# Kernel tuning notes

Hardware: AMD Instinct MI355X
Metric: run time of the kernel (lower is better)

The kernel has to match this reference:

```python
import jax, jax.numpy as jnp
import numpy as np

N_NODES = 10000
N_EDGES = 160000
IN_DIM = 256
HEADS = 8
C0 = 32   # per-head out channels, layer 0 (256 // 8)
C1 = 32   # per-head out channels, layer 1 (= output_dim)
RANK = 8
LORA_SCALE = 32.0 / 8      # alpha / rank
ATT_RANK = 4               # rank // 2
ATT_SCALE = 32.0 / 4       # alpha / (rank // 2)
NEG_SLOPE = 0.2


def _gat_layer(x, src, dst, W, A, B, att_s, att_d, As, Bs, Ad, Bd, concat):
    """One LoRAGATConv layer (eval mode, dropout=0)."""
    N = x.shape[0]
    H, C = att_s.shape
    # LoRA-adapted projection: base + B(A x) * scaling -> [N, H, C]
    xp = (x @ W.T + ((x @ A.T) @ B.T) * LORA_SCALE).reshape(N, H, C)

    def att_score(base, Aa, Ba):
        # per-head base dot product + LoRA(out_channels -> 1) path -> [N, H]
        return jnp.einsum('nhc,hc->nh', xp, base) + ((xp @ Aa.T) @ Ba.T)[..., 0] * ATT_SCALE

    s_src = att_score(att_s, As, Bs)  # applied to x_i (destination), per original code
    s_dst = att_score(att_d, Ad, Bd)  # applied to x_j (source), per original code

    alpha = s_src[dst] + s_dst[src]              # [E, H]
    alpha = jax.nn.leaky_relu(alpha, NEG_SLOPE)
    # segment softmax over destination nodes (every node has a self-loop)
    m = jax.ops.segment_max(alpha, dst, num_segments=N)
    e = jnp.exp(alpha - m[dst])
    den = jax.ops.segment_sum(e, dst, num_segments=N)
    a = e / den[dst]                             # [E, H]

    msg = xp[src] * a[:, :, None]                # [E, H, C]
    out = jax.ops.segment_sum(msg, dst, num_segments=N)  # [N, H, C]
    return out.reshape(N, H * C) if concat else out.mean(axis=1)


def _forward(x, edge_index,
             W0, A0, B0, att_src0, att_dst0, Asrc0, Bsrc0, Adst0, Bdst0,
             W1, A1, B1, att_src1, att_dst1, Asrc1, Bsrc1, Adst1, Bdst1):
    N = x.shape[0]
    loops = jnp.arange(N, dtype=edge_index.dtype)
    ei = jnp.concatenate([edge_index, jnp.stack([loops, loops])], axis=1)
    src, dst = ei[0], ei[1]
    h = _gat_layer(x, src, dst, W0, A0, B0, att_src0, att_dst0, Asrc0, Bsrc0, Adst0, Bdst0, concat=True)
    h = jax.nn.elu(h)
    out = _gat_layer(h, src, dst, W1, A1, B1, att_src1, att_dst1, Asrc1, Bsrc1, Adst1, Bdst1, concat=False)
    return out


def setup_inputs() -> dict:
    key = jax.random.key(0)
    ks = jax.random.split(key, 24)
    s = 0.05
    inp = {
        'x': jax.random.normal(ks[0], (N_NODES, IN_DIM), dtype=jnp.float32),
        'edge_index': jax.random.randint(ks[1], (2, N_EDGES), 0, N_NODES, dtype=jnp.int64),
    }
    # layer 0: in 256 -> heads*C0 = 256
    inp['W0'] = jax.random.normal(ks[2], (HEADS * C0, IN_DIM), dtype=jnp.float32) * s
    inp['A0'] = jax.random.normal(ks[3], (RANK, IN_DIM), dtype=jnp.float32) * s
    inp['B0'] = jax.random.normal(ks[4], (HEADS * C0, RANK), dtype=jnp.float32) * s
    inp['att_src0'] = jax.random.normal(ks[5], (HEADS, C0), dtype=jnp.float32) * s
    inp['att_dst0'] = jax.random.normal(ks[6], (HEADS, C0), dtype=jnp.float32) * s
    inp['Asrc0'] = jax.random.normal(ks[7], (ATT_RANK, C0), dtype=jnp.float32) * s
    inp['Bsrc0'] = jax.random.normal(ks[8], (1, ATT_RANK), dtype=jnp.float32) * s
    inp['Adst0'] = jax.random.normal(ks[9], (ATT_RANK, C0), dtype=jnp.float32) * s
    inp['Bdst0'] = jax.random.normal(ks[10], (1, ATT_RANK), dtype=jnp.float32) * s
    # layer 1: in heads*C0 = 256 -> heads*C1 = 256 (head-averaged -> 32)
    D1 = HEADS * C0
    inp['W1'] = jax.random.normal(ks[11], (HEADS * C1, D1), dtype=jnp.float32) * s
    inp['A1'] = jax.random.normal(ks[12], (RANK, D1), dtype=jnp.float32) * s
    inp['B1'] = jax.random.normal(ks[13], (HEADS * C1, RANK), dtype=jnp.float32) * s
    inp['att_src1'] = jax.random.normal(ks[14], (HEADS, C1), dtype=jnp.float32) * s
    inp['att_dst1'] = jax.random.normal(ks[15], (HEADS, C1), dtype=jnp.float32) * s
    inp['Asrc1'] = jax.random.normal(ks[16], (ATT_RANK, C1), dtype=jnp.float32) * s
    inp['Bsrc1'] = jax.random.normal(ks[17], (1, ATT_RANK), dtype=jnp.float32) * s
    inp['Adst1'] = jax.random.normal(ks[18], (ATT_RANK, C1), dtype=jnp.float32) * s
    inp['Bdst1'] = jax.random.normal(ks[19], (1, ATT_RANK), dtype=jnp.float32) * s
    return inp


def reference(x, edge_index,
              W0, A0, B0, att_src0, att_dst0, Asrc0, Bsrc0, Adst0, Bdst0,
              W1, A1, B1, att_src1, att_dst1, Asrc1, Bsrc1, Adst1, Bdst1):
    return _forward(x, edge_index,
                    W0, A0, B0, att_src0, att_dst0, Asrc0, Bsrc0, Adst0, Bdst0,
                    W1, A1, B1, att_src1, att_dst1, Asrc1, Bsrc1, Adst1, Bdst1)
```

## Files before the change

### kernel.cpp

```cpp
#include <hip/hip_runtime.h>

#define LORA_SCALE 4.0f
#define ATT_SCALE 8.0f
#define NEG_SLOPE 0.2f
#define ELLW 64

typedef __attribute__((ext_vector_type(8))) short bf16x8;
typedef __attribute__((ext_vector_type(4))) float f32x4;
typedef unsigned short ushort_t;
typedef unsigned int uint_t;

__device__ inline ushort_t f2bf(float f) {
    uint_t u = __float_as_uint(f);
    u += 0x7fff + ((u >> 16) & 1);
    return (ushort_t)(u >> 16);
}
__device__ inline float bf2f(ushort_t h) {
    return __uint_as_float(((uint_t)h) << 16);
}
__device__ inline void split_bf(float f, ushort_t& h, ushort_t& l) {
    h = f2bf(f);
    l = f2bf(f - bf2f(h));
}

__global__ void prep_all(const float* __restrict__ W0, const float* __restrict__ A0,
                         const float* __restrict__ B0,
                         const float* __restrict__ att_s0, const float* __restrict__ att_d0,
                         const float* __restrict__ As0, const float* __restrict__ Bs0,
                         const float* __restrict__ Ad0, const float* __restrict__ Bd0,
                         const float* __restrict__ W1, const float* __restrict__ A1,
                         const float* __restrict__ B1,
                         const float* __restrict__ att_s1, const float* __restrict__ att_d1,
                         const float* __restrict__ As1, const float* __restrict__ Bs1,
                         const float* __restrict__ Ad1, const float* __restrict__ Bd1,
                         ushort_t* __restrict__ whi0, ushort_t* __restrict__ wlo0,
                         ushort_t* __restrict__ whi1, ushort_t* __restrict__ wlo1,
                         float* __restrict__ effS0, float* __restrict__ effD0,
                         float* __restrict__ effS1, float* __restrict__ effD1,
                         const float* __restrict__ x, ushort_t* __restrict__ xhi,
                         ushort_t* __restrict__ xlo,
                         const int* __restrict__ ei, int E_real, int E_total,
                         int* __restrict__ cnt, int* __restrict__ ell, int N)
{
    int b = blockIdx.x;
    int t = threadIdx.x;
    if (b < 512) {
        int layer = b >> 8;
        int i = (b & 255) * 256 + t;
        const float* W = layer ? W1 : W0;
        const float* A = layer ? A1 : A0;
        const float* B = layer ? B1 : B0;
        int r = i >> 8, c = i & 255;
        float acc = W[i];
        #pragma unroll
        for (int k = 0; k < 8; k++) acc += LORA_SCALE * B[r * 8 + k] * A[k * 256 + c];
        ushort_t h, l;
        split_bf(acc, h, l);
        if (layer) { whi1[i] = h; wlo1[i] = l; }
        else       { whi0[i] = h; wlo0[i] = l; }
        if (i < 256) {
            int c2 = i & 31;
            const float* as_ = layer ? att_s1 : att_s0;
            const float* ad_ = layer ? att_d1 : att_d0;
            const float* As = layer ? As1 : As0;
            const float* Bs = layer ? Bs1 : Bs0;
            const float* Ad = layer ? Ad1 : Ad0;
            const float* Bd = layer ? Bd1 : Bd0;
            float es = as_[i], ed = ad_[i];
            #pragma unroll
            for (int k = 0; k < 4; k++) {
                es += ATT_SCALE * Bs[k] * As[k * 32 + c2];
                ed += ATT_SCALE * Bd[k] * Ad[k * 32 + c2];
            }
            if (layer) { effS1[i] = es; effD1[i] = ed; }
            else       { effS0[i] = es; effD0[i] = ed; }
        }
        return;
    }
    int cb = b - 512;
    int convB = (N * 32 + 255) / 256;
    if (cb < convB) {
        int i = cb * 256 + t;
        if (i >= N * 32) return;
        float4 v0 = *(const float4*)(x + i * 8);
        float4 v1 = *(const float4*)(x + i * 8 + 4);
        ushort4 h0, l0, h1, l1;
        split_bf(v0.x, h0.x, l0.x);
        split_bf(v0.y, h0.y, l0.y);
        split_bf(v0.z, h0.z, l0.z);
        split_bf(v0.w, h0.w, l0.w);
        split_bf(v1.x, h1.x, l1.x);
        split_bf(v1.y, h1.y, l1.y);
        split_bf(v1.z, h1.z, l1.z);
        split_bf(v1.w, h1.w, l1.w);
        *(ushort4*)(xhi + i * 8) = h0;
        *(ushort4*)(xhi + i * 8 + 4) = h1;
        *(ushort4*)(xlo + i * 8) = l0;
        *(ushort4*)(xlo + i * 8 + 4) = l1;
        return;
    }
    int e = (cb - convB) * 256 + t;
    if (e >= E_total) return;
    int s, d;
    if (e < E_real) { s = ei[e]; d = ei[E_real + e]; }
    else            { s = d = e - E_real; }
    int pos = atomicAdd(&cnt[d], 1);
    if (pos < ELLW) ell[d * ELLW + pos] = s;
}

__global__ __launch_bounds__(512) void gemm_fused(
    const ushort_t* __restrict__ Ahi, const ushort_t* __restrict__ Alo,
    const ushort_t* __restrict__ Bhi, const ushort_t* __restrict__ Blo,
    const float* __restrict__ effS, const float* __restrict__ effD,
    ushort_t* __restrict__ Cb, float* __restrict__ ssrc, float* __restrict__ sdst, int M)
{
    __shared__ ushort_t sBh[16384];
    __shared__ ushort_t sBl[16384];
    const int K = 256;
    int tid = threadIdx.x;
    int n0 = blockIdx.x * 64;

    const ushort_t* srcH = Bhi + (size_t)n0 * K;
    const ushort_t* srcL = Blo + (size_t)n0 * K;
    #pragma unroll
    for (int c = 0; c < 4; c++) {
        int g  = c * 512 + tid;
        int rr = g >> 5;
        int ch = g & 31;
        int kblk = ch >> 2, quad = ch & 3;
        int tt = rr >> 4, l16r = rr & 15;
        int dst = (((tt * 8 + kblk) * 4 + quad) * 16 + l16r) * 8;
        *(bf16x8*)&sBh[dst] = *(const bf16x8*)(srcH + rr * K + ch * 8);
        *(bf16x8*)&sBl[dst] = *(const bf16x8*)(srcL + rr * K + ch * 8);
    }
    __syncthreads();

    int w = tid >> 6;
    int lane = tid & 63;
    int quad = lane >> 4;
    int l16 = lane & 15;
    int m0 = blockIdx.y * 128 + w * 16;
    int mr = m0 + l16; if (mr >= M) mr = M - 1;

    const ushort_t* ah = Ahi + mr * K + quad * 8;
    const ushort_t* al = Alo + mr * K + quad * 8;

    f32x4 acc[4] = {};
    #pragma unroll
    for (int kb = 0; kb < 8; kb++) {
        bf16x8 a_hi = *(const bf16x8*)(ah + kb * 32);
        bf16x8 a_lo = *(const bf16x8*)(al + kb * 32);
        #pragma unroll
        for (int t = 0; t < 4; t++) {
            int off = (((t * 8 + kb) * 4 + quad) * 16 + l16) * 8;
            bf16x8 b_hi = *(const bf16x8*)&sBh[off];
            bf16x8 b_lo = *(const bf16x8*)&sBl[off];
            acc[t] = __builtin_amdgcn_mfma_f32_16x16x32_bf16(a_hi, b_hi, acc[t], 0, 0, 0);
            acc[t] = __builtin_amdgcn_mfma_f32_16x16x32_bf16(a_hi, b_lo, acc[t], 0, 0, 0);
            acc[t] = __builtin_amdgcn_mfma_f32_16x16x32_bf16(a_lo, b_hi, acc[t], 0, 0, 0);
        }
    }

    #pragma unroll
    for (int t = 0; t < 4; t++) {
        #pragma unroll
        for (int r = 0; r < 4; r++) {
            int m = m0 + quad * 4 + r;
            if (m < M) Cb[m * 256 + n0 + t * 16 + l16] = f2bf(acc[t][r]);
        }
    }

    int h0 = n0 >> 5;
    float vs[2][4], vd[2][4];
    #pragma unroll
    for (int g = 0; g < 2; g++) {
        float e0s = effS[n0 + 32 * g + l16];
        float e1s = effS[n0 + 32 * g + 16 + l16];
        float e0d = effD[n0 + 32 * g + l16];
        float e1d = effD[n0 + 32 * g + 16 + l16];
        #pragma unroll
        for (int r = 0; r < 4; r++) {
            vs[g][r] = acc[2 * g][r] * e0s + acc[2 * g + 1][r] * e1s;
            vd[g][r] = acc[2 * g][r] * e0d + acc[2 * g + 1][r] * e1d;
        }
    }
    #pragma unroll
    for (int m = 1; m <= 8; m <<= 1) {
        #pragma unroll
        for (int g = 0; g < 2; g++)
            #pragma unroll
            for (int r = 0; r < 4; r++) {
                vs[g][r] += __shfl_xor(vs[g][r], m);
                vd[g][r] += __shfl_xor(vd[g][r], m);
            }
    }
    if (l16 == 0) {
        #pragma unroll
        for (int g = 0; g < 2; g++)
            #pragma unroll
            for (int r = 0; r < 4; r++) {
                int m = m0 + quad * 4 + r;
                if (m < M) {
                    ssrc[m * 8 + h0 + g] = vs[g][r];
                    sdst[m * 8 + h0 + g] = vd[g][r];
                }
            }
    }
}

__global__ __launch_bounds__(256) void ell_agg(const int* __restrict__ cnt,
                                               const int* __restrict__ ell,
                                               const ushort_t* __restrict__ xpb,
                                               const float* __restrict__ ssrc,
                                               const float* __restrict__ sdst,
                                               float* __restrict__ out,
                                               ushort_t* __restrict__ ohi,
                                               ushort_t* __restrict__ olo,
                                               int N, int mode)
{
    __shared__ int sidx[4][ELLW];
    int gid = blockIdx.x * blockDim.x + threadIdx.x;
    int d = gid >> 6;
    if (d >= N) return;
    int w = threadIdx.x >> 6;
    int lane = threadIdx.x & 63;
    int eo = lane >> 5;
    int l32 = lane & 31;
    int h = l32 >> 2;
    float ssrc_h = ssrc[d * 8 + h];
    int end = cnt[d]; if (end > ELLW) end = ELLW;
    const int* row = ell + d * ELLW;
    sidx[w][lane] = row[lane < end ? lane : 0];

    float acc[8] = {};
    float den = 0.f;
    for (int i = 0; i < end; i += 8) {
        int idx[4];
        #pragma unroll
        for (int p = 0; p < 4; p++) {
            int ii = i + 2 * p + eo;
            idx[p] = sidx[w][ii < end ? ii : 0];
        }
        float t4[4];
        #pragma unroll
        for (int p = 0; p < 4; p++) t4[p] = sdst[idx[p] * 8 + h];
        bf16x8 v[4];
        #pragma unroll
        for (int p = 0; p < 4; p++)
            v[p] = *(const bf16x8*)(xpb + idx[p] * 256 + l32 * 8);
        #pragma unroll
        for (int p = 0; p < 4; p++) {
            int ii = i + 2 * p + eo;
            float al = ssrc_h + t4[p];
            al = al > 0.f ? al : NEG_SLOPE * al;
            float wgt = (ii < end) ? __expf(al) : 0.f;
            den += wgt;
            #pragma unroll
            for (int j = 0; j < 8; j++)
                acc[j] += bf2f((ushort_t)v[p][j]) * wgt;
        }
    }
    #pragma unroll
    for (int j = 0; j < 8; j++) acc[j] += __shfl_xor(acc[j], 32);
    den += __shfl_xor(den, 32);
    float inv = 1.f / den;
    #pragma unroll
    for (int j = 0; j < 8; j++) acc[j] *= inv;

    if (mode == 2) {
        #pragma unroll
        for (int m = 4; m <= 16; m <<= 1)
            #pragma unroll
            for (int j = 0; j < 8; j++) acc[j] += __shfl_xor(acc[j], m);
        if (lane < 4) {
            float4 r0 = { acc[0] * 0.125f, acc[1] * 0.125f, acc[2] * 0.125f, acc[3] * 0.125f };
            float4 r1 = { acc[4] * 0.125f, acc[5] * 0.125f, acc[6] * 0.125f, acc[7] * 0.125f };
            *(float4*)(out + d * 32 + l32 * 8) = r0;
            *(float4*)(out + d * 32 + l32 * 8 + 4) = r1;
        }
        return;
    }
    #pragma unroll
    for (int j = 0; j < 8; j++)
        acc[j] = acc[j] > 0.f ? acc[j] : (__expf(acc[j]) - 1.f);
    if (eo == 0) {
        ushort_t hs[8], ls[8];
        #pragma unroll
        for (int j = 0; j < 8; j++) split_bf(acc[j], hs[j], ls[j]);
        *(ushort4*)(ohi + d * 256 + l32 * 8)     = *(ushort4*)&hs[0];
        *(ushort4*)(ohi + d * 256 + l32 * 8 + 4) = *(ushort4*)&hs[4];
        *(ushort4*)(olo + d * 256 + l32 * 8)     = *(ushort4*)&ls[0];
        *(ushort4*)(olo + d * 256 + l32 * 8 + 4) = *(ushort4*)&ls[4];
    }
}

extern "C" void kernel_launch(void* const* d_in, const int* in_sizes, int n_in,
                              void* d_out, int out_size, void* d_ws, size_t ws_size,
                              hipStream_t stream)
{
    const float* x  = (const float*)d_in[0];
    const int*   ei = (const int*)d_in[1];
    const float* W0 = (const float*)d_in[2];
    const float* A0 = (const float*)d_in[3];
    const float* B0 = (const float*)d_in[4];
    const float* att_s0 = (const float*)d_in[5];
    const float* att_d0 = (const float*)d_in[6];
    const float* As0 = (const float*)d_in[7];
    const float* Bs0 = (const float*)d_in[8];
    const float* Ad0 = (const float*)d_in[9];
    const float* Bd0 = (const float*)d_in[10];
    const float* W1 = (const float*)d_in[11];
    const float* A1 = (const float*)d_in[12];
    const float* B1 = (const float*)d_in[13];
    const float* att_s1 = (const float*)d_in[14];
    const float* att_d1 = (const float*)d_in[15];
    const float* As1 = (const float*)d_in[16];
    const float* Bs1 = (const float*)d_in[17];
    const float* Ad1 = (const float*)d_in[18];
    const float* Bd1 = (const float*)d_in[19];

    const int N = in_sizes[0] / 256;
    const int E_real = in_sizes[1] / 2;
    const int E_total = E_real + N;

    ushort_t* whi0 = (ushort_t*)d_ws;
    ushort_t* wlo0 = whi0 + 65536;
    ushort_t* whi1 = wlo0 + 65536;
    ushort_t* wlo1 = whi1 + 65536;
    ushort_t* xhi  = wlo1 + 65536;
    ushort_t* xlo  = xhi + 2560000;
    ushort_t* hbhi = xlo + 2560000;
    ushort_t* hblo = hbhi + 2560000;
    ushort_t* xpb  = hblo + 2560000;
    float* effS0 = (float*)(xpb + 2560000);
    float* effD0 = effS0 + 256;
    float* effS1 = effD0 + 256;
    float* effD1 = effS1 + 256;
    float* ssrc  = effD1 + 256;
    float* sdst  = ssrc + 80000;
    int* cnt = (int*)(sdst + 80000);
    int* ell = cnt + 10016;

    hipMemsetAsync(cnt, 0, (size_t)N * sizeof(int), stream);
    int convB = (N * 32 + 255) / 256;
    int fillB = (E_total + 255) / 256;
    prep_all<<<512 + convB + fillB, 256, 0, stream>>>(
        W0, A0, B0, att_s0, att_d0, As0, Bs0, Ad0, Bd0,
        W1, A1, B1, att_s1, att_d1, As1, Bs1, Ad1, Bd1,
        whi0, wlo0, whi1, wlo1, effS0, effD0, effS1, effD1,
        x, xhi, xlo, ei, E_real, E_total, cnt, ell, N);

    dim3 gg(4, (N + 127) / 128);
    int aggBlocks = (N * 64 + 255) / 256;

    gemm_fused<<<gg, 512, 0, stream>>>(xhi, xlo, whi0, wlo0, effS0, effD0, xpb, ssrc, sdst, N);
    ell_agg<<<aggBlocks, 256, 0, stream>>>(cnt, ell, xpb, ssrc, sdst,
                                           nullptr, hbhi, hblo, N, 1);

    gemm_fused<<<gg, 512, 0, stream>>>(hbhi, hblo, whi1, wlo1, effS1, effD1, xpb, ssrc, sdst, N);
    ell_agg<<<aggBlocks, 256, 0, stream>>>(cnt, ell, xpb, ssrc, sdst,
                                           (float*)d_out, nullptr, nullptr, N, 2);
}
```

Measured before the change: 167.6 us.

## Merge all stages into one cooperative persistent kernel with grid syncs

Replaces the memset and five kernel launches (prep, two GEMMs, two aggregations) with a single cooperative kernel. Stages are separated by grid-wide barriers and use grid-stride and tile loops. The goal is to remove per-launch overhead and the gaps between kernels. In exchange the grid is capped at up to 512 blocks of 512 threads, which can lower parallelism in the aggregation phases and adds the cost of each grid barrier.

```diff
diff --git a/kernel.cpp b/kernel.cpp
--- a/kernel.cpp
+++ b/kernel.cpp
@@ -1,4 +1,7 @@
 #include <hip/hip_runtime.h>
+#include <hip/hip_cooperative_groups.h>
+
+namespace cg = cooperative_groups;
 
 #define LORA_SCALE 4.0f
 #define ATT_SCALE 8.0f
@@ -23,301 +26,327 @@
     l = f2bf(f - bf2f(h));
 }
 
-__global__ void prep_all(const float* __restrict__ W0, const float* __restrict__ A0,
-                         const float* __restrict__ B0,
-                         const float* __restrict__ att_s0, const float* __restrict__ att_d0,
-                         const float* __restrict__ As0, const float* __restrict__ Bs0,
-                         const float* __restrict__ Ad0, const float* __restrict__ Bd0,
-                         const float* __restrict__ W1, const float* __restrict__ A1,
-                         const float* __restrict__ B1,
-                         const float* __restrict__ att_s1, const float* __restrict__ att_d1,
-                         const float* __restrict__ As1, const float* __restrict__ Bs1,
-                         const float* __restrict__ Ad1, const float* __restrict__ Bd1,
-                         ushort_t* __restrict__ whi0, ushort_t* __restrict__ wlo0,
-                         ushort_t* __restrict__ whi1, ushort_t* __restrict__ wlo1,
-                         float* __restrict__ effS0, float* __restrict__ effD0,
-                         float* __restrict__ effS1, float* __restrict__ effD1,
-                         const float* __restrict__ x, ushort_t* __restrict__ xhi,
-                         ushort_t* __restrict__ xlo,
-                         const int* __restrict__ ei, int E_real, int E_total,
-                         int* __restrict__ cnt, int* __restrict__ ell, int N)
+struct MegaParams {
+    const float *W0, *A0, *B0, *att_s0, *att_d0, *As0, *Bs0, *Ad0, *Bd0;
+    const float *W1, *A1, *B1, *att_s1, *att_d1, *As1, *Bs1, *Ad1, *Bd1;
+    const float *x;
+    const int *ei;
+    ushort_t *whi0, *wlo0, *whi1, *wlo1;
+    ushort_t *xhi, *xlo, *hbhi, *hblo, *xpb;
+    float *effS0, *effD0, *effS1, *effD1;
+    float *ssrc, *sdst;
+    int *cnt, *ell;
+    float *out;
+    int N, E_real, E_total, nTiles;
+};
+
+__device__ void gemm_phase(const ushort_t* __restrict__ Ahi, const ushort_t* __restrict__ Alo,
+                           const ushort_t* __restrict__ Bhi, const ushort_t* __restrict__ Blo,
+                           const float* __restrict__ effS, const float* __restrict__ effD,
+                           ushort_t* __restrict__ Cb, float* __restrict__ ssrc,
+                           float* __restrict__ sdst, int M, int nTiles,
+                           ushort_t* sBh, ushort_t* sBl)
 {
-    int b = blockIdx.x;
-    int t = threadIdx.x;
-    if (b < 512) {
-        int layer = b >> 8;
-        int i = (b & 255) * 256 + t;
-        const float* W = layer ? W1 : W0;
-        const float* A = layer ? A1 : A0;
-        const float* B = layer ? B1 : B0;
-        int r = i >> 8, c = i & 255;
-        float acc = W[i];
-        #pragma unroll
-        for (int k = 0; k < 8; k++) acc += LORA_SCALE * B[r * 8 + k] * A[k * 256 + c];
-        ushort_t h, l;
-        split_bf(acc, h, l);
-        if (layer) { whi1[i] = h; wlo1[i] = l; }
-        else       { whi0[i] = h; wlo0[i] = l; }
-        if (i < 256) {
-            int c2 = i & 31;
-            const float* as_ = layer ? att_s1 : att_s0;
-            const float* ad_ = layer ? att_d1 : att_d0;
-            const float* As = layer ? As1 : As0;
-            const float* Bs = layer ? Bs1 : Bs0;
-            const float* Ad = layer ? Ad1 : Ad0;
-            const float* Bd = layer ? Bd1 : Bd0;
-            float es = as_[i], ed = ad_[i];
-            #pragma unroll
-            for (int k = 0; k < 4; k++) {
-                es += ATT_SCALE * Bs[k] * As[k * 32 + c2];
-                ed += ATT_SCALE * Bd[k] * Ad[k * 32 + c2];
-            }
-            if (layer) { effS1[i] = es; effD1[i] = ed; }
-            else       { effS0[i] = es; effD0[i] = ed; }
-        }
-        return;
-    }
-    int cb = b - 512;
-    int convB = (N * 32 + 255) / 256;
-    if (cb < convB) {
-        int i = cb * 256 + t;
-        if (i >= N * 32) return;
-        float4 v0 = *(const float4*)(x + i * 8);
-        float4 v1 = *(const float4*)(x + i * 8 + 4);
-        ushort4 h0, l0, h1, l1;
-        split_bf(v0.x, h0.x, l0.x);
-        split_bf(v0.y, h0.y, l0.y);
-        split_bf(v0.z, h0.z, l0.z);
-        split_bf(v0.w, h0.w, l0.w);
-        split_bf(v1.x, h1.x, l1.x);
-        split_bf(v1.y, h1.y, l1.y);
-        split_bf(v1.z, h1.z, l1.z);
-        split_bf(v1.w, h1.w, l1.w);
-        *(ushort4*)(xhi + i * 8) = h0;
-        *(ushort4*)(xhi + i * 8 + 4) = h1;
-        *(ushort4*)(xlo + i * 8) = l0;
-        *(ushort4*)(xlo + i * 8 + 4) = l1;
-        return;
-    }
-    int e = (cb - convB) * 256 + t;
-    if (e >= E_total) return;
-    int s, d;
-    if (e < E_real) { s = ei[e]; d = ei[E_real + e]; }
-    else            { s = d = e - E_real; }
-    int pos = atomicAdd(&cnt[d], 1);
-    if (pos < ELLW) ell[d * ELLW + pos] = s;
-}
-
-__global__ __launch_bounds__(512) void gemm_fused(
-    const ushort_t* __restrict__ Ahi, const ushort_t* __restrict__ Alo,
-    const ushort_t* __restrict__ Bhi, const ushort_t* __restrict__ Blo,
-    const float* __restrict__ effS, const float* __restrict__ effD,
-    ushort_t* __restrict__ Cb, float* __restrict__ ssrc, float* __restrict__ sdst, int M)
-{
-    __shared__ ushort_t sBh[16384];
-    __shared__ ushort_t sBl[16384];
     const int K = 256;
     int tid = threadIdx.x;
-    int n0 = blockIdx.x * 64;
-
-    const ushort_t* srcH = Bhi + (size_t)n0 * K;
-    const ushort_t* srcL = Blo + (size_t)n0 * K;
-    #pragma unroll
-    for (int c = 0; c < 4; c++) {
-        int g  = c * 512 + tid;
-        int rr = g >> 5;
-        int ch = g & 31;
-        int kblk = ch >> 2, quad = ch & 3;
-        int tt = rr >> 4, l16r = rr & 15;
-        int dst = (((tt * 8 + kblk) * 4 + quad) * 16 + l16r) * 8;
-        *(bf16x8*)&sBh[dst] = *(const bf16x8*)(srcH + rr * K + ch * 8);
-        *(bf16x8*)&sBl[dst] = *(const bf16x8*)(srcL + rr * K + ch * 8);
-    }
-    __syncthreads();
-
     int w = tid >> 6;
     int lane = tid & 63;
     int quad = lane >> 4;
     int l16 = lane & 15;
-    int m0 = blockIdx.y * 128 + w * 16;
-    int mr = m0 + l16; if (mr >= M) mr = M - 1;
-
-    const ushort_t* ah = Ahi + mr * K + quad * 8;
-    const ushort_t* al = Alo + mr * K + quad * 8;
-
-    f32x4 acc[4] = {};
-    #pragma unroll
-    for (int kb = 0; kb < 8; kb++) {
-        bf16x8 a_hi = *(const bf16x8*)(ah + kb * 32);
-        bf16x8 a_lo = *(const bf16x8*)(al + kb * 32);
+
+    for (int tile = blockIdx.x; tile < nTiles; tile += gridDim.x) {
+        int n0 = (tile & 3) * 64;
+        int m0 = (tile >> 2) * 128 + w * 16;
+
+        const ushort_t* srcH = Bhi + (size_t)n0 * K;
+        const ushort_t* srcL = Blo + (size_t)n0 * K;
+        #pragma unroll
+        for (int c = 0; c < 4; c++) {
+            int g  = c * 512 + tid;
+            int rr = g >> 5;
+            int ch = g & 31;
+            int kblk = ch >> 2, qd = ch & 3;
+            int tt = rr >> 4, l16r = rr & 15;
+            int dst = (((tt * 8 + kblk) * 4 + qd) * 16 + l16r) * 8;
+            *(bf16x8*)&sBh[dst] = *(const bf16x8*)(srcH + rr * K + ch * 8);
+            *(bf16x8*)&sBl[dst] = *(const bf16x8*)(srcL + rr * K + ch * 8);
+        }
+        __syncthreads();
+
+        int mr = m0 + l16; if (mr >= M) mr = M - 1;
+        const ushort_t* ah = Ahi + mr * K + quad * 8;
+        const ushort_t* al = Alo + mr * K + quad * 8;
+
+        f32x4 acc[4] = {};
+        #pragma unroll
+        for (int kb = 0; kb < 8; kb++) {
+            bf16x8 a_hi = *(const bf16x8*)(ah + kb * 32);
+            bf16x8 a_lo = *(const bf16x8*)(al + kb * 32);
+            #pragma unroll
+            for (int t = 0; t < 4; t++) {
+                int off = (((t * 8 + kb) * 4 + quad) * 16 + l16) * 8;
+                bf16x8 b_hi = *(const bf16x8*)&sBh[off];
+                bf16x8 b_lo = *(const bf16x8*)&sBl[off];
+                acc[t] = __builtin_amdgcn_mfma_f32_16x16x32_bf16(a_hi, b_hi, acc[t], 0, 0, 0);
+                acc[t] = __builtin_amdgcn_mfma_f32_16x16x32_bf16(a_hi, b_lo, acc[t], 0, 0, 0);
+                acc[t] = __builtin_amdgcn_mfma_f32_16x16x32_bf16(a_lo, b_hi, acc[t], 0, 0, 0);
+            }
+        }
+
         #pragma unroll
         for (int t = 0; t < 4; t++) {
-            int off = (((t * 8 + kb) * 4 + quad) * 16 + l16) * 8;
-            bf16x8 b_hi = *(const bf16x8*)&sBh[off];
-            bf16x8 b_lo = *(const bf16x8*)&sBl[off];
-            acc[t] = __builtin_amdgcn_mfma_f32_16x16x32_bf16(a_hi, b_hi, acc[t], 0, 0, 0);
-            acc[t] = __builtin_amdgcn_mfma_f32_16x16x32_bf16(a_hi, b_lo, acc[t], 0, 0, 0);
-            acc[t] = __builtin_amdgcn_mfma_f32_16x16x32_bf16(a_lo, b_hi, acc[t], 0, 0, 0);
-        }
-    }
-
-    #pragma unroll
-    for (int t = 0; t < 4; t++) {
-        #pragma unroll
-        for (int r = 0; r < 4; r++) {
-            int m = m0 + quad * 4 + r;
-            if (m < M) Cb[m * 256 + n0 + t * 16 + l16] = f2bf(acc[t][r]);
-        }
-    }
-
-    int h0 = n0 >> 5;
-    float vs[2][4], vd[2][4];
-    #pragma unroll
-    for (int g = 0; g < 2; g++) {
-        float e0s = effS[n0 + 32 * g + l16];
-        float e1s = effS[n0 + 32 * g + 16 + l16];
-        float e0d = effD[n0 + 32 * g + l16];
-        float e1d = effD[n0 + 32 * g + 16 + l16];
-        #pragma unroll
-        for (int r = 0; r < 4; r++) {
-            vs[g][r] = acc[2 * g][r] * e0s + acc[2 * g + 1][r] * e1s;
-            vd[g][r] = acc[2 * g][r] * e0d + acc[2 * g + 1][r] * e1d;
-        }
-    }
-    #pragma unroll
-    for (int m = 1; m <= 8; m <<= 1) {
-        #pragma unroll
-        for (int g = 0; g < 2; g++)
-            #pragma unroll
-            for (int r = 0; r < 4; r++) {
-                vs[g][r] += __shfl_xor(vs[g][r], m);
-                vd[g][r] += __shfl_xor(vd[g][r], m);
-            }
-    }
-    if (l16 == 0) {
-        #pragma unroll
-        for (int g = 0; g < 2; g++)
             #pragma unroll
             for (int r = 0; r < 4; r++) {
                 int m = m0 + quad * 4 + r;
-                if (m < M) {
-                    ssrc[m * 8 + h0 + g] = vs[g][r];
-                    sdst[m * 8 + h0 + g] = vd[g][r];
+                if (m < M) Cb[m * 256 + n0 + t * 16 + l16] = f2bf(acc[t][r]);
+            }
+        }
+
+        int h0 = n0 >> 5;
+        float vs[2][4], vd[2][4];
+        #pragma unroll
+        for (int g = 0; g < 2; g++) {
+            float e0s = effS[n0 + 32 * g + l16];
+            float e1s = effS[n0 + 32 * g + 16 + l16];
+            float e0d = effD[n0 + 32 * g + l16];
+            float e1d = effD[n0 + 32 * g + 16 + l16];
+            #pragma unroll
+            for (int r = 0; r < 4; r++) {
+                vs[g][r] = acc[2 * g][r] * e0s + acc[2 * g + 1][r] * e1s;
+                vd[g][r] = acc[2 * g][r] * e0d + acc[2 * g + 1][r] * e1d;
+            }
+        }
+        #pragma unroll
+        for (int m = 1; m <= 8; m <<= 1) {
+            #pragma unroll
+            for (int g = 0; g < 2; g++)
+                #pragma unroll
+                for (int r = 0; r < 4; r++) {
+                    vs[g][r] += __shfl_xor(vs[g][r], m);
+                    vd[g][r] += __shfl_xor(vd[g][r], m);
                 }
-            }
+        }
+        if (l16 == 0) {
+            #pragma unroll
+            for (int g = 0; g < 2; g++)
+                #pragma unroll
+                for (int r = 0; r < 4; r++) {
+                    int m = m0 + quad * 4 + r;
+                    if (m < M) {
+                        ssrc[m * 8 + h0 + g] = vs[g][r];
+                        sdst[m * 8 + h0 + g] = vd[g][r];
+                    }
+                }
+        }
+        __syncthreads();
     }
 }
 
-__global__ __launch_bounds__(256) void ell_agg(const int* __restrict__ cnt,
-                                               const int* __restrict__ ell,
-                                               const ushort_t* __restrict__ xpb,
-                                               const float* __restrict__ ssrc,
-                                               const float* __restrict__ sdst,
-                                               float* __restrict__ out,
-                                               ushort_t* __restrict__ ohi,
-                                               ushort_t* __restrict__ olo,
-                                               int N, int mode)
+__device__ void agg_phase(const int* __restrict__ cnt, const int* __restrict__ ell,
+                          const ushort_t* __restrict__ xpb,
+                          const float* __restrict__ ssrc, const float* __restrict__ sdst,
+                          float* __restrict__ out, ushort_t* __restrict__ ohi,
+                          ushort_t* __restrict__ olo, int N, int mode, int* sidx)
 {
-    __shared__ int sidx[4][ELLW];
-    int gid = blockIdx.x * blockDim.x + threadIdx.x;
-    int d = gid >> 6;
-    if (d >= N) return;
     int w = threadIdx.x >> 6;
     int lane = threadIdx.x & 63;
     int eo = lane >> 5;
     int l32 = lane & 31;
     int h = l32 >> 2;
-    float ssrc_h = ssrc[d * 8 + h];
-    int end = cnt[d]; if (end > ELLW) end = ELLW;
-    const int* row = ell + d * ELLW;
-    sidx[w][lane] = row[lane < end ? lane : 0];
-
-    float acc[8] = {};
-    float den = 0.f;
-    for (int i = 0; i < end; i += 8) {
-        int idx[4];
-        #pragma unroll
-        for (int p = 0; p < 4; p++) {
-            int ii = i + 2 * p + eo;
-            idx[p] = sidx[w][ii < end ? ii : 0];
-        }
-        float t4[4];
-        #pragma unroll
-        for (int p = 0; p < 4; p++) t4[p] = sdst[idx[p] * 8 + h];
-        bf16x8 v[4];
-        #pragma unroll
-        for (int p = 0; p < 4; p++)
-            v[p] = *(const bf16x8*)(xpb + idx[p] * 256 + l32 * 8);
-        #pragma unroll
-        for (int p = 0; p < 4; p++) {
-            int ii = i + 2 * p + eo;
-            float al = ssrc_h + t4[p];
-            al = al > 0.f ? al : NEG_SLOPE * al;
-            float wgt = (ii < end) ? __expf(al) : 0.f;
-            den += wgt;
+    int* srow = sidx + w * ELLW;
+    int groups = (N + 7) >> 3;
+
+    for (int g = blockIdx.x; g < groups; g += gridDim.x) {
+        int d = g * 8 + w;
+        if (d >= N) continue;
+        float ssrc_h = ssrc[d * 8 + h];
+        int end = cnt[d]; if (end > ELLW) end = ELLW;
+        const int* row = ell + d * ELLW;
+        srow[lane] = row[lane < end ? lane : 0];
+
+        float acc[8] = {};
+        float den = 0.f;
+        for (int i = 0; i < end; i += 8) {
+            int idx[4];
+            #pragma unroll
+            for (int pp = 0; pp < 4; pp++) {
+                int ii = i + 2 * pp + eo;
+                idx[pp] = srow[ii < end ? ii : 0];
+            }
+            float t4[4];
+            #pragma unroll
+            for (int pp = 0; pp < 4; pp++) t4[pp] = sdst[idx[pp] * 8 + h];
+            bf16x8 v[4];
+            #pragma unroll
+            for (int pp = 0; pp < 4; pp++)
+                v[pp] = *(const bf16x8*)(xpb + idx[pp] * 256 + l32 * 8);
+            #pragma unroll
+            for (int pp = 0; pp < 4; pp++) {
+                int ii = i + 2 * pp + eo;
+                float al = ssrc_h + t4[pp];
+                al = al > 0.f ? al : NEG_SLOPE * al;
+                float wgt = (ii < end) ? __expf(al) : 0.f;
+                den += wgt;
+                #pragma unroll
+                for (int j = 0; j < 8; j++)
+                    acc[j] += bf2f((ushort_t)v[pp][j]) * wgt;
+            }
+        }
+        #pragma unroll
+        for (int j = 0; j < 8; j++) acc[j] += __shfl_xor(acc[j], 32);
+        den += __shfl_xor(den, 32);
+        float inv = 1.f / den;
+        #pragma unroll
+        for (int j = 0; j < 8; j++) acc[j] *= inv;
+
+        if (mode == 2) {
+            #pragma unroll
+            for (int m = 4; m <= 16; m <<= 1)
+                #pragma unroll
+                for (int j = 0; j < 8; j++) acc[j] += __shfl_xor(acc[j], m);
+            if (lane < 4) {
+                float4 r0 = { acc[0] * 0.125f, acc[1] * 0.125f, acc[2] * 0.125f, acc[3] * 0.125f };
+                float4 r1 = { acc[4] * 0.125f, acc[5] * 0.125f, acc[6] * 0.125f, acc[7] * 0.125f };
+                *(float4*)(out + d * 32 + l32 * 8) = r0;
+                *(float4*)(out + d * 32 + l32 * 8 + 4) = r1;
+            }
+        } else {
             #pragma unroll
             for (int j = 0; j < 8; j++)
-                acc[j] += bf2f((ushort_t)v[p][j]) * wgt;
+                acc[j] = acc[j] > 0.f ? acc[j] : (__expf(acc[j]) - 1.f);
+            if (eo == 0) {
+                ushort_t hs[8], ls[8];
+                #pragma unroll
+                for (int j = 0; j < 8; j++) split_bf(acc[j], hs[j], ls[j]);
+                *(ushort4*)(ohi + d * 256 + l32 * 8)     = *(ushort4*)&hs[0];
+                *(ushort4*)(ohi + d * 256 + l32 * 8 + 4) = *(ushort4*)&hs[4];
+                *(ushort4*)(olo + d * 256 + l32 * 8)     = *(ushort4*)&ls[0];
+                *(ushort4*)(olo + d * 256 + l32 * 8 + 4) = *(ushort4*)&ls[4];
+            }
         }
     }
-    #pragma unroll
-    for (int j = 0; j < 8; j++) acc[j] += __shfl_xor(acc[j], 32);
-    den += __shfl_xor(den, 32);
-    float inv = 1.f / den;
-    #pragma unroll
-    for (int j = 0; j < 8; j++) acc[j] *= inv;
-
-    if (mode == 2) {
-        #pragma unroll
-        for (int m = 4; m <= 16; m <<= 1)
-            #pragma unroll
-            for (int j = 0; j < 8; j++) acc[j] += __shfl_xor(acc[j], m);
-        if (lane < 4) {
-            float4 r0 = { acc[0] * 0.125f, acc[1] * 0.125f, acc[2] * 0.125f, acc[3] * 0.125f };
-            float4 r1 = { acc[4] * 0.125f, acc[5] * 0.125f, acc[6] * 0.125f, acc[7] * 0.125f };
-            *(float4*)(out + d * 32 + l32 * 8) = r0;
-            *(float4*)(out + d * 32 + l32 * 8 + 4) = r1;
-        }
-        return;
+}
+
+__global__ __launch_bounds__(512, 4) void mega(MegaParams p)
+{
+    __shared__ ushort_t sBh[16384];
+    __shared__ ushort_t sBl[16384];
+    cg::grid_group grid = cg::this_grid();
+
+    int tid = threadIdx.x;
+    int gtid = blockIdx.x * 512 + tid;
+    int gsize = gridDim.x * 512;
+    int N = p.N;
+
+    const int U0 = 131072;
+    const int U1 = U0 + 512;
+    const int U2 = U1 + N * 32;
+    const int U3 = U2 + N;
+    for (int u = gtid; u < U3; u += gsize) {
+        if (u < U0) {
+            int layer = u >> 16;
+            int i = u & 65535;
+            const float* W = layer ? p.W1 : p.W0;
+            const float* A = layer ? p.A1 : p.A0;
+            const float* B = layer ? p.B1 : p.B0;
+            int r = i >> 8, c = i & 255;
+            float acc = W[i];
+            #pragma unroll
+            for (int k = 0; k < 8; k++) acc += LORA_SCALE * B[r * 8 + k] * A[k * 256 + c];
+            ushort_t hh, ll;
+            split_bf(acc, hh, ll);
+            if (layer) { p.whi1[i] = hh; p.wlo1[i] = ll; }
+            else       { p.whi0[i] = hh; p.wlo0[i] = ll; }
+        } else if (u < U1) {
+            int v = u - U0;
+            int layer = v >> 8;
+            int i = v & 255;
+            int c2 = i & 31;
+            const float* as_ = layer ? p.att_s1 : p.att_s0;
+            const float* ad_ = layer ? p.att_d1 : p.att_d0;
+            const float* As = layer ? p.As1 : p.As0;
+            const float* Bs = layer ? p.Bs1 : p.Bs0;
+            const float* Ad = layer ? p.Ad1 : p.Ad0;
+            const float* Bd = layer ? p.Bd1 : p.Bd0;
+            float es = as_[i], ed = ad_[i];
+            #pragma unroll
+            for (int k = 0; k < 4; k++) {
+                es += ATT_SCALE * Bs[k] * As[k * 32 + c2];
+                ed += ATT_SCALE * Bd[k] * Ad[k * 32 + c2];
+            }
+            if (layer) { p.effS1[i] = es; p.effD1[i] = ed; }
+            else       { p.effS0[i] = es; p.effD0[i] = ed; }
+        } else if (u < U2) {
+            int i = u - U1;
+            float4 v0 = *(const float4*)(p.x + (size_t)i * 8);
+            float4 v1 = *(const float4*)(p.x + (size_t)i * 8 + 4);
+            ushort4 h0, l0, h1, l1;
+            split_bf(v0.x, h0.x, l0.x);
+            split_bf(v0.y, h0.y, l0.y);
+            split_bf(v0.z, h0.z, l0.z);
+            split_bf(v0.w, h0.w, l0.w);
+            split_bf(v1.x, h1.x, l1.x);
+            split_bf(v1.y, h1.y, l1.y);
+            split_bf(v1.z, h1.z, l1.z);
+            split_bf(v1.w, h1.w, l1.w);
+            *(ushort4*)(p.xhi + (size_t)i * 8)     = h0;
+            *(ushort4*)(p.xhi + (size_t)i * 8 + 4) = h1;
+            *(ushort4*)(p.xlo + (size_t)i * 8)     = l0;
+            *(ushort4*)(p.xlo + (size_t)i * 8 + 4) = l1;
+        } else {
+            p.cnt[u - U2] = 0;
+        }
     }
-    #pragma unroll
-    for (int j = 0; j < 8; j++)
-        acc[j] = acc[j] > 0.f ? acc[j] : (__expf(acc[j]) - 1.f);
-    if (eo == 0) {
-        ushort_t hs[8], ls[8];
-        #pragma unroll
-        for (int j = 0; j < 8; j++) split_bf(acc[j], hs[j], ls[j]);
-        *(ushort4*)(ohi + d * 256 + l32 * 8)     = *(ushort4*)&hs[0];
-        *(ushort4*)(ohi + d * 256 + l32 * 8 + 4) = *(ushort4*)&hs[4];
-        *(ushort4*)(olo + d * 256 + l32 * 8)     = *(ushort4*)&ls[0];
-        *(ushort4*)(olo + d * 256 + l32 * 8 + 4) = *(ushort4*)&ls[4];
+    grid.sync();
+
+    for (int e = gtid; e < p.E_total; e += gsize) {
+        int s, d;
+        if (e < p.E_real) { s = p.ei[e]; d = p.ei[p.E_real + e]; }
+        else              { s = d = e - p.E_real; }
+        int pos = atomicAdd(&p.cnt[d], 1);
+        if (pos < ELLW) p.ell[d * ELLW + pos] = s;
     }
+    grid.sync();
+
+    gemm_phase(p.xhi, p.xlo, p.whi0, p.wlo0, p.effS0, p.effD0,
+               p.xpb, p.ssrc, p.sdst, N, p.nTiles, sBh, sBl);
+    grid.sync();
+    agg_phase(p.cnt, p.ell, p.xpb, p.ssrc, p.sdst,
+              nullptr, p.hbhi, p.hblo, N, 1, (int*)sBh);
+    grid.sync();
+
+    gemm_phase(p.hbhi, p.hblo, p.whi1, p.wlo1, p.effS1, p.effD1,
+               p.xpb, p.ssrc, p.sdst, N, p.nTiles, sBh, sBl);
+    grid.sync();
+    agg_phase(p.cnt, p.ell, p.xpb, p.ssrc, p.sdst,
+              p.out, nullptr, nullptr, N, 2, (int*)sBh);
 }
 
 extern "C" void kernel_launch(void* const* d_in, const int* in_sizes, int n_in,
                               void* d_out, int out_size, void* d_ws, size_t ws_size,
                               hipStream_t stream)
 {
-    const float* x  = (const float*)d_in[0];
-    const int*   ei = (const int*)d_in[1];
-    const float* W0 = (const float*)d_in[2];
-    const float* A0 = (const float*)d_in[3];
-    const float* B0 = (const float*)d_in[4];
-    const float* att_s0 = (const float*)d_in[5];
-    const float* att_d0 = (const float*)d_in[6];
-    const float* As0 = (const float*)d_in[7];
-    const float* Bs0 = (const float*)d_in[8];
-    const float* Ad0 = (const float*)d_in[9];
-    const float* Bd0 = (const float*)d_in[10];
-    const float* W1 = (const float*)d_in[11];
-    const float* A1 = (const float*)d_in[12];
-    const float* B1 = (const float*)d_in[13];
-    const float* att_s1 = (const float*)d_in[14];
-    const float* att_d1 = (const float*)d_in[15];
-    const float* As1 = (const float*)d_in[16];
-    const float* Bs1 = (const float*)d_in[17];
-    const float* Ad1 = (const float*)d_in[18];
-    const float* Bd1 = (const float*)d_in[19];
+    MegaParams p;
+    p.x  = (const float*)d_in[0];
+    p.ei = (const int*)d_in[1];
+    p.W0 = (const float*)d_in[2];
+    p.A0 = (const float*)d_in[3];
+    p.B0 = (const float*)d_in[4];
+    p.att_s0 = (const float*)d_in[5];
+    p.att_d0 = (const float*)d_in[6];
+    p.As0 = (const float*)d_in[7];
+    p.Bs0 = (const float*)d_in[8];
+    p.Ad0 = (const float*)d_in[9];
+    p.Bd0 = (const float*)d_in[10];
+    p.W1 = (const float*)d_in[11];
+    p.A1 = (const float*)d_in[12];
+    p.B1 = (const float*)d_in[13];
+    p.att_s1 = (const float*)d_in[14];
+    p.att_d1 = (const float*)d_in[15];
+    p.As1 = (const float*)d_in[16];
+    p.Bs1 = (const float*)d_in[17];
+    p.Ad1 = (const float*)d_in[18];
+    p.Bd1 = (const float*)d_in[19];
 
     const int N = in_sizes[0] / 256;
     const int E_real = in_sizes[1] / 2;
@@ -341,23 +370,20 @@
     int* cnt = (int*)(sdst + 80000);
     int* ell = cnt + 10016;
 
-    hipMemsetAsync(cnt, 0, (size_t)N * sizeof(int), stream);
-    int convB = (N * 32 + 255) / 256;
-    int fillB = (E_total + 255) / 256;
-    prep_all<<<512 + convB + fillB, 256, 0, stream>>>(
-        W0, A0, B0, att_s0, att_d0, As0, Bs0, Ad0, Bd0,
-        W1, A1, B1, att_s1, att_d1, As1, Bs1, Ad1, Bd1,
-        whi0, wlo0, whi1, wlo1, effS0, effD0, effS1, effD1,
-        x, xhi, xlo, ei, E_real, E_total, cnt, ell, N);
-
-    dim3 gg(4, (N + 127) / 128);
-    int aggBlocks = (N * 64 + 255) / 256;
-
-    gemm_fused<<<gg, 512, 0, stream>>>(xhi, xlo, whi0, wlo0, effS0, effD0, xpb, ssrc, sdst, N);
-    ell_agg<<<aggBlocks, 256, 0, stream>>>(cnt, ell, xpb, ssrc, sdst,
-                                           nullptr, hbhi, hblo, N, 1);
-
-    gemm_fused<<<gg, 512, 0, stream>>>(hbhi, hblo, whi1, wlo1, effS1, effD1, xpb, ssrc, sdst, N);
-    ell_agg<<<aggBlocks, 256, 0, stream>>>(cnt, ell, xpb, ssrc, sdst,
-                                           (float*)d_out, nullptr, nullptr, N, 2);
-}
+    p.whi0 = whi0; p.wlo0 = wlo0; p.whi1 = whi1; p.wlo1 = wlo1;
+    p.xhi = xhi; p.xlo = xlo; p.hbhi = hbhi; p.hblo = hblo; p.xpb = xpb;
+    p.effS0 = effS0; p.effD0 = effD0; p.effS1 = effS1; p.effD1 = effD1;
+    p.ssrc = ssrc; p.sdst = sdst; p.cnt = cnt; p.ell = ell;
+    p.out = (float*)d_out;
+    p.N = N; p.E_real = E_real; p.E_total = E_total;
+    p.nTiles = 4 * ((N + 127) / 128);
+
+    int occ = 0;
+    hipOccupancyMaxActiveBlocksPerMultiprocessor(&occ, (const void*)mega, 512, 0);
+    if (occ < 1) occ = 1;
+    int grid = occ * 256;
+    if (grid > 512) grid = 512;
+
+    void* args[] = { (void*)&p };
+    hipLaunchCooperativeKernel((const void*)mega, dim3(grid), dim3(512), args, 0, stream);
+}
```

Result: slower. 381.0 us (+127.4%).

## Fold weight prep and input bf16 split into GEMM, drop prep kernel and memset

Applied to the files above, without the earlier changes.

Removes the prep kernel that precomputed LoRA-merged split weights and converted x into hi/lo bf16 buffers. The GEMM now builds the merged weight tile in shared memory from W/A/B per block, and in layer 0 splits fp32 x on the fly. The layer-0 GEMM also zeroes the degree counters, which replaces the memset. The ELL fill becomes its own kernel that runs after the first GEMM. This cuts the x hi/lo round-trip through memory and one launch, at the cost of recomputing the LoRA merge in every block.

```diff
diff --git a/kernel.cpp b/kernel.cpp
--- a/kernel.cpp
+++ b/kernel.cpp
@@ -23,83 +23,10 @@
     l = f2bf(f - bf2f(h));
 }
 
-__global__ void prep_all(const float* __restrict__ W0, const float* __restrict__ A0,
-                         const float* __restrict__ B0,
-                         const float* __restrict__ att_s0, const float* __restrict__ att_d0,
-                         const float* __restrict__ As0, const float* __restrict__ Bs0,
-                         const float* __restrict__ Ad0, const float* __restrict__ Bd0,
-                         const float* __restrict__ W1, const float* __restrict__ A1,
-                         const float* __restrict__ B1,
-                         const float* __restrict__ att_s1, const float* __restrict__ att_d1,
-                         const float* __restrict__ As1, const float* __restrict__ Bs1,
-                         const float* __restrict__ Ad1, const float* __restrict__ Bd1,
-                         ushort_t* __restrict__ whi0, ushort_t* __restrict__ wlo0,
-                         ushort_t* __restrict__ whi1, ushort_t* __restrict__ wlo1,
-                         float* __restrict__ effS0, float* __restrict__ effD0,
-                         float* __restrict__ effS1, float* __restrict__ effD1,
-                         const float* __restrict__ x, ushort_t* __restrict__ xhi,
-                         ushort_t* __restrict__ xlo,
-                         const int* __restrict__ ei, int E_real, int E_total,
-                         int* __restrict__ cnt, int* __restrict__ ell, int N)
+__global__ void ell_fill(const int* __restrict__ ei, int E_real, int E_total,
+                         int* __restrict__ cnt, int* __restrict__ ell)
 {
-    int b = blockIdx.x;
-    int t = threadIdx.x;
-    if (b < 512) {
-        int layer = b >> 8;
-        int i = (b & 255) * 256 + t;
-        const float* W = layer ? W1 : W0;
-        const float* A = layer ? A1 : A0;
-        const float* B = layer ? B1 : B0;
-        int r = i >> 8, c = i & 255;
-        float acc = W[i];
-        #pragma unroll
-        for (int k = 0; k < 8; k++) acc += LORA_SCALE * B[r * 8 + k] * A[k * 256 + c];
-        ushort_t h, l;
-        split_bf(acc, h, l);
-        if (layer) { whi1[i] = h; wlo1[i] = l; }
-        else       { whi0[i] = h; wlo0[i] = l; }
-        if (i < 256) {
-            int c2 = i & 31;
-            const float* as_ = layer ? att_s1 : att_s0;
-            const float* ad_ = layer ? att_d1 : att_d0;
-            const float* As = layer ? As1 : As0;
-            const float* Bs = layer ? Bs1 : Bs0;
-            const float* Ad = layer ? Ad1 : Ad0;
-            const float* Bd = layer ? Bd1 : Bd0;
-            float es = as_[i], ed = ad_[i];
-            #pragma unroll
-            for (int k = 0; k < 4; k++) {
-                es += ATT_SCALE * Bs[k] * As[k * 32 + c2];
-                ed += ATT_SCALE * Bd[k] * Ad[k * 32 + c2];
-            }
-            if (layer) { effS1[i] = es; effD1[i] = ed; }
-            else       { effS0[i] = es; effD0[i] = ed; }
-        }
-        return;
-    }
-    int cb = b - 512;
-    int convB = (N * 32 + 255) / 256;
-    if (cb < convB) {
-        int i = cb * 256 + t;
-        if (i >= N * 32) return;
-        float4 v0 = *(const float4*)(x + i * 8);
-        float4 v1 = *(const float4*)(x + i * 8 + 4);
-        ushort4 h0, l0, h1, l1;
-        split_bf(v0.x, h0.x, l0.x);
-        split_bf(v0.y, h0.y, l0.y);
-        split_bf(v0.z, h0.z, l0.z);
-        split_bf(v0.w, h0.w, l0.w);
-        split_bf(v1.x, h1.x, l1.x);
-        split_bf(v1.y, h1.y, l1.y);
-        split_bf(v1.z, h1.z, l1.z);
-        split_bf(v1.w, h1.w, l1.w);
-        *(ushort4*)(xhi + i * 8) = h0;
-        *(ushort4*)(xhi + i * 8 + 4) = h1;
-        *(ushort4*)(xlo + i * 8) = l0;
-        *(ushort4*)(xlo + i * 8 + 4) = l1;
-        return;
-    }
-    int e = (cb - convB) * 256 + t;
+    int e = blockIdx.x * 256 + threadIdx.x;
     if (e >= E_total) return;
     int s, d;
     if (e < E_real) { s = ei[e]; d = ei[E_real + e]; }
@@ -108,11 +35,17 @@
     if (pos < ELLW) ell[d * ELLW + pos] = s;
 }
 
-__global__ __launch_bounds__(512) void gemm_fused(
+template<int MODE>
+__global__ __launch_bounds__(512, 4) void gemm_fused(
+    const float* __restrict__ Xf,
     const ushort_t* __restrict__ Ahi, const ushort_t* __restrict__ Alo,
-    const ushort_t* __restrict__ Bhi, const ushort_t* __restrict__ Blo,
-    const float* __restrict__ effS, const float* __restrict__ effD,
-    ushort_t* __restrict__ Cb, float* __restrict__ ssrc, float* __restrict__ sdst, int M)
+    const float* __restrict__ W, const float* __restrict__ Alora,
+    const float* __restrict__ Blora,
+    const float* __restrict__ att_s, const float* __restrict__ att_d,
+    const float* __restrict__ As, const float* __restrict__ Bs,
+    const float* __restrict__ Ad, const float* __restrict__ Bd,
+    ushort_t* __restrict__ Cb, float* __restrict__ ssrc, float* __restrict__ sdst,
+    int* __restrict__ cnt, int M)
 {
     __shared__ ushort_t sBh[16384];
     __shared__ ushort_t sBl[16384];
@@ -120,18 +53,45 @@
     int tid = threadIdx.x;
     int n0 = blockIdx.x * 64;
 
-    const ushort_t* srcH = Bhi + (size_t)n0 * K;
-    const ushort_t* srcL = Blo + (size_t)n0 * K;
+    if (MODE == 0) {
+        int bid = blockIdx.y * 4 + blockIdx.x;
+        if (bid < 40) {
+            int i = bid * 256 + tid;
+            if (i < 10240) cnt[i] = 0;
+        }
+    }
+
     #pragma unroll
     for (int c = 0; c < 4; c++) {
         int g  = c * 512 + tid;
         int rr = g >> 5;
         int ch = g & 31;
-        int kblk = ch >> 2, quad = ch & 3;
+        int gr = n0 + rr;
+        const float* wrow = W + gr * 256 + ch * 8;
+        const float* brow = Blora + gr * 8;
+        float a8[8];
+        #pragma unroll
+        for (int j = 0; j < 8; j++) a8[j] = wrow[j];
+        #pragma unroll
+        for (int k = 0; k < 8; k++) {
+            float bv = LORA_SCALE * brow[k];
+            const float* arow = Alora + k * 256 + ch * 8;
+            #pragma unroll
+            for (int j = 0; j < 8; j++) a8[j] += bv * arow[j];
+        }
+        bf16x8 vh, vl;
+        #pragma unroll
+        for (int j = 0; j < 8; j++) {
+            ushort_t hh, ll;
+            split_bf(a8[j], hh, ll);
+            vh[j] = (short)hh;
+            vl[j] = (short)ll;
+        }
+        int kblk = ch >> 2, qd = ch & 3;
         int tt = rr >> 4, l16r = rr & 15;
-        int dst = (((tt * 8 + kblk) * 4 + quad) * 16 + l16r) * 8;
-        *(bf16x8*)&sBh[dst] = *(const bf16x8*)(srcH + rr * K + ch * 8);
-        *(bf16x8*)&sBl[dst] = *(const bf16x8*)(srcL + rr * K + ch * 8);
+        int dst = (((tt * 8 + kblk) * 4 + qd) * 16 + l16r) * 8;
+        *(bf16x8*)&sBh[dst] = vh;
+        *(bf16x8*)&sBl[dst] = vl;
     }
     __syncthreads();
 
@@ -142,14 +102,29 @@
     int m0 = blockIdx.y * 128 + w * 16;
     int mr = m0 + l16; if (mr >= M) mr = M - 1;
 
-    const ushort_t* ah = Ahi + mr * K + quad * 8;
-    const ushort_t* al = Alo + mr * K + quad * 8;
+    const float* xrow = (MODE == 0) ? (Xf + (size_t)mr * K + quad * 8) : nullptr;
+    const ushort_t* ah = (MODE == 1) ? (Ahi + (size_t)mr * K + quad * 8) : nullptr;
+    const ushort_t* al = (MODE == 1) ? (Alo + (size_t)mr * K + quad * 8) : nullptr;
 
     f32x4 acc[4] = {};
     #pragma unroll
     for (int kb = 0; kb < 8; kb++) {
-        bf16x8 a_hi = *(const bf16x8*)(ah + kb * 32);
-        bf16x8 a_lo = *(const bf16x8*)(al + kb * 32);
+        bf16x8 a_hi, a_lo;
+        if (MODE == 0) {
+            float4 f0 = *(const float4*)(xrow + kb * 32);
+            float4 f1 = *(const float4*)(xrow + kb * 32 + 4);
+            float fv[8] = { f0.x, f0.y, f0.z, f0.w, f1.x, f1.y, f1.z, f1.w };
+            #pragma unroll
+            for (int j = 0; j < 8; j++) {
+                ushort_t hh, ll;
+                split_bf(fv[j], hh, ll);
+                a_hi[j] = (short)hh;
+                a_lo[j] = (short)ll;
+            }
+        } else {
+            a_hi = *(const bf16x8*)(ah + kb * 32);
+            a_lo = *(const bf16x8*)(al + kb * 32);
+        }
         #pragma unroll
         for (int t = 0; t < 4; t++) {
             int off = (((t * 8 + kb) * 4 + quad) * 16 + l16) * 8;
@@ -174,10 +149,16 @@
     float vs[2][4], vd[2][4];
     #pragma unroll
     for (int g = 0; g < 2; g++) {
-        float e0s = effS[n0 + 32 * g + l16];
-        float e1s = effS[n0 + 32 * g + 16 + l16];
-        float e0d = effD[n0 + 32 * g + l16];
-        float e1d = effD[n0 + 32 * g + 16 + l16];
+        int cA = n0 + 32 * g + l16;
+        float e0s = att_s[cA],      e0d = att_d[cA];
+        float e1s = att_s[cA + 16], e1d = att_d[cA + 16];
+        #pragma unroll
+        for (int k = 0; k < 4; k++) {
+            e0s += ATT_SCALE * Bs[k] * As[k * 32 + l16];
+            e1s += ATT_SCALE * Bs[k] * As[k * 32 + 16 + l16];
+            e0d += ATT_SCALE * Bd[k] * Ad[k * 32 + l16];
+            e1d += ATT_SCALE * Bd[k] * Ad[k * 32 + 16 + l16];
+        }
         #pragma unroll
         for (int r = 0; r < 4; r++) {
             vs[g][r] = acc[2 * g][r] * e0s + acc[2 * g + 1][r] * e1s;
@@ -237,27 +218,27 @@
     for (int i = 0; i < end; i += 8) {
         int idx[4];
         #pragma unroll
-        for (int p = 0; p < 4; p++) {
-            int ii = i + 2 * p + eo;
-            idx[p] = sidx[w][ii < end ? ii : 0];
+        for (int pp = 0; pp < 4; pp++) {
+            int ii = i + 2 * pp + eo;
+            idx[pp] = sidx[w][ii < end ? ii : 0];
         }
         float t4[4];
         #pragma unroll
-        for (int p = 0; p < 4; p++) t4[p] = sdst[idx[p] * 8 + h];
+        for (int pp = 0; pp < 4; pp++) t4[pp] = sdst[idx[pp] * 8 + h];
         bf16x8 v[4];
         #pragma unroll
-        for (int p = 0; p < 4; p++)
-            v[p] = *(const bf16x8*)(xpb + idx[p] * 256 + l32 * 8);
-        #pragma unroll
-        for (int p = 0; p < 4; p++) {
-            int ii = i + 2 * p + eo;
-            float al = ssrc_h + t4[p];
+        for (int pp = 0; pp < 4; pp++)
+            v[pp] = *(const bf16x8*)(xpb + idx[pp] * 256 + l32 * 8);
+        #pragma unroll
+        for (int pp = 0; pp < 4; pp++) {
+            int ii = i + 2 * pp + eo;
+            float al = ssrc_h + t4[pp];
             al = al > 0.f ? al : NEG_SLOPE * al;
             float wgt = (ii < end) ? __expf(al) : 0.f;
             den += wgt;
             #pragma unroll
             for (int j = 0; j < 8; j++)
-                acc[j] += bf2f((ushort_t)v[p][j]) * wgt;
+                acc[j] += bf2f((ushort_t)v[pp][j]) * wgt;
         }
     }
     #pragma unroll
@@ -323,41 +304,30 @@
     const int E_real = in_sizes[1] / 2;
     const int E_total = E_real + N;
 
-    ushort_t* whi0 = (ushort_t*)d_ws;
-    ushort_t* wlo0 = whi0 + 65536;
-    ushort_t* whi1 = wlo0 + 65536;
-    ushort_t* wlo1 = whi1 + 65536;
-    ushort_t* xhi  = wlo1 + 65536;
-    ushort_t* xlo  = xhi + 2560000;
-    ushort_t* hbhi = xlo + 2560000;
+    ushort_t* hbhi = (ushort_t*)d_ws;
     ushort_t* hblo = hbhi + 2560000;
     ushort_t* xpb  = hblo + 2560000;
-    float* effS0 = (float*)(xpb + 2560000);
-    float* effD0 = effS0 + 256;
-    float* effS1 = effD0 + 256;
-    float* effD1 = effS1 + 256;
-    float* ssrc  = effD1 + 256;
-    float* sdst  = ssrc + 80000;
+    float* ssrc = (float*)(xpb + 2560000);
+    float* sdst = ssrc + 80000;
     int* cnt = (int*)(sdst + 80000);
-    int* ell = cnt + 10016;
-
-    hipMemsetAsync(cnt, 0, (size_t)N * sizeof(int), stream);
-    int convB = (N * 32 + 255) / 256;
+    int* ell = cnt + 10240;
+
+    dim3 gg(4, (N + 127) / 128);
     int fillB = (E_total + 255) / 256;
-    prep_all<<<512 + convB + fillB, 256, 0, stream>>>(
+    int aggBlocks = (N * 64 + 255) / 256;
+
+    gemm_fused<0><<<gg, 512, 0, stream>>>(
+        x, nullptr, nullptr,
         W0, A0, B0, att_s0, att_d0, As0, Bs0, Ad0, Bd0,
-        W1, A1, B1, att_s1, att_d1, As1, Bs1, Ad1, Bd1,
-        whi0, wlo0, whi1, wlo1, effS0, effD0, effS1, effD1,
-        x, xhi, xlo, ei, E_real, E_total, cnt, ell, N);
-
-    dim3 gg(4, (N + 127) / 128);
-    int aggBlocks = (N * 64 + 255) / 256;
-
-    gemm_fused<<<gg, 512, 0, stream>>>(xhi, xlo, whi0, wlo0, effS0, effD0, xpb, ssrc, sdst, N);
+        xpb, ssrc, sdst, cnt, N);
+    ell_fill<<<fillB, 256, 0, stream>>>(ei, E_real, E_total, cnt, ell);
     ell_agg<<<aggBlocks, 256, 0, stream>>>(cnt, ell, xpb, ssrc, sdst,
                                            nullptr, hbhi, hblo, N, 1);
 
-    gemm_fused<<<gg, 512, 0, stream>>>(hbhi, hblo, whi1, wlo1, effS1, effD1, xpb, ssrc, sdst, N);
+    gemm_fused<1><<<gg, 512, 0, stream>>>(
+        nullptr, hbhi, hblo,
+        W1, A1, B1, att_s1, att_d1, As1, Bs1, Ad1, Bd1,
+        xpb, ssrc, sdst, nullptr, N);
     ell_agg<<<aggBlocks, 256, 0, stream>>>(cnt, ell, xpb, ssrc, sdst,
                                            (float*)d_out, nullptr, nullptr, N, 2);
 }
```

New measurement: 182.7 us. 9.0% more time.
